# Optimization experiments

Hardware: AMD Instinct MI355X
Metric: run time of the kernel (lower is better)

The kernel has to match this reference:

```python
import jax, jax.numpy as jnp
import numpy as np

B, N, M, H, NH, IN, OUT = 64, 8192, 128, 512, 2, 128, 128
CTRL_IN = IN + NH * M  # 384


def setup_inputs() -> dict:
    key = jax.random.key(0)
    ks = jax.random.split(key, 20)
    d = {}
    d["x"] = jax.random.normal(ks[0], (B, IN), jnp.float32)
    d["prev_reads"] = jax.random.normal(ks[1], (NH, B, M), jnp.float32)
    d["h0"] = jax.random.normal(ks[2], (B, H), jnp.float32) * 0.1
    d["c0"] = jax.random.normal(ks[3], (B, H), jnp.float32) * 0.1
    wr = jax.random.uniform(ks[4], (NH, B, N), jnp.float32)
    ww = jax.random.uniform(ks[5], (NH, B, N), jnp.float32)
    d["prev_w_read"] = wr / jnp.sum(wr, axis=-1, keepdims=True)
    d["prev_w_write"] = ww / jnp.sum(ww, axis=-1, keepdims=True)
    d["memory"] = jax.random.normal(ks[6], (B, N, M), jnp.float32) * 0.1
    d["W_ih"] = jax.random.normal(ks[7], (4 * H, CTRL_IN), jnp.float32) * 0.02
    d["W_hh"] = jax.random.normal(ks[8], (4 * H, H), jnp.float32) * 0.02
    d["b_ih"] = jnp.zeros((4 * H,), jnp.float32)
    d["b_hh"] = jnp.zeros((4 * H,), jnp.float32)
    d["Wr"] = jax.random.normal(ks[9], (NH, M + 6, H), jnp.float32) * 0.05
    d["br"] = jnp.zeros((NH, M + 6), jnp.float32)
    d["Ww"] = jax.random.normal(ks[10], (NH, 3 * M + 6, H), jnp.float32) * 0.05
    d["bw"] = jnp.zeros((NH, 3 * M + 6), jnp.float32)
    d["fc_W"] = jax.random.normal(ks[11], (OUT, NH * M), jnp.float32) * 0.05
    d["fc_b"] = jnp.zeros((OUT,), jnp.float32)
    return d


def _lstm_cell(x, h, c, W_ih, W_hh, b_ih, b_hh):
    gates = x @ W_ih.T + b_ih + h @ W_hh.T + b_hh
    i, f, g, o = jnp.split(gates, 4, axis=1)  # torch gate order i,f,g,o
    i, f, o = jax.nn.sigmoid(i), jax.nn.sigmoid(f), jax.nn.sigmoid(o)
    c_new = f * c + i * jnp.tanh(g)
    return o * jnp.tanh(c_new), c_new


def _address(mem, k, beta, g, s, gamma, w_prev):
    # content addressing: cosine similarity (torch eps = 1e-8 on each norm)
    mem_e = mem + 1e-16
    k_e = k + 1e-16
    num = jnp.einsum('bnm,bm->bn', mem_e, k_e)
    den = jnp.maximum(jnp.linalg.norm(mem_e, axis=-1), 1e-8) * \
          jnp.maximum(jnp.linalg.norm(k_e, axis=-1), 1e-8)[:, None]
    wc = jax.nn.softmax(beta * num / den, axis=1)
    # interpolation
    wg = g * wc + (1.0 - g) * w_prev
    # circular convolution with 3-tap shift kernel s
    wt = s[:, 0:1] * jnp.roll(wg, 1, axis=1) + s[:, 1:2] * wg + s[:, 2:3] * jnp.roll(wg, -1, axis=1)
    # sharpening
    wp = wt ** gamma
    return wp / (jnp.sum(wp, axis=1, keepdims=True) + 1e-16)


def _split_params(o, m):
    k = o[:, :m]
    beta = jax.nn.softplus(o[:, m:m + 1])
    g = jax.nn.sigmoid(o[:, m + 1:m + 2])
    s = jax.nn.softmax(o[:, m + 2:m + 5], axis=1)
    gamma = 1.0 + jax.nn.softplus(o[:, m + 5:m + 6])
    return k, beta, g, s, gamma


def reference(x, prev_reads, h0, c0, prev_w_read, prev_w_write, memory,
              W_ih, W_hh, b_ih, b_hh, Wr, br, Ww, bw, fc_W, fc_b):
    nh, b, m = prev_reads.shape
    # controller input: [x, r_0, ..., r_{nh-1}]
    inp = jnp.concatenate([x, jnp.transpose(prev_reads, (1, 0, 2)).reshape(b, nh * m)], axis=1)
    ctrl_out, c_new = _lstm_cell(inp, h0, c0, W_ih, W_hh, b_ih, b_hh)
    reads = []
    mem = memory
    for i in range(nh):  # heads interleaved [read_i, write_i]; writes mutate memory
        # read head i
        ro = ctrl_out @ Wr[i].T + br[i]
        k, beta, g, s, gamma = _split_params(ro, m)
        w_r = _address(mem, k, beta, g, s, gamma, prev_w_read[i])
        reads.append(jnp.einsum('bn,bnm->bm', w_r, mem))
        # write head i
        wo = ctrl_out @ Ww[i].T + bw[i]
        k, beta, g, s, gamma = _split_params(wo, m)
        e = jax.nn.sigmoid(wo[:, m + 6:2 * m + 6])
        a = wo[:, 2 * m + 6:3 * m + 6]
        w_w = _address(mem, k, beta, g, s, gamma, prev_w_write[i])
        mem = mem * (1.0 - w_w[:, :, None] * e[:, None, :]) + w_w[:, :, None] * a[:, None, :]
    inp2 = jnp.concatenate(reads, axis=1)
    o = jax.nn.sigmoid(inp2 @ fc_W.T + fc_b)
    return o
```

## Files before the change

kernel.cpp:

```cpp
#include <hip/hip_runtime.h>

#define BB 64
#define NN 8192
#define MM 128
#define HH 512
#define KLSTM 896
#define JTOT 2048
#define COLS 658
#define OUTN 128
#define CHUNKS 32
#define PROW 388
#define RSTR 672

__device__ __forceinline__ float sigf(float x){ return 1.0f/(1.0f+__expf(-x)); }
__device__ __forceinline__ float tanhf_f(float x){ return 1.0f - 2.0f/(__expf(2.0f*x)+1.0f); }
__device__ __forceinline__ float softplusf_(float x){ return (x>20.0f)? x : log1pf(expf(x)); }

__global__ __launch_bounds__(128) void k_lstm_split(
    const float* __restrict__ x, const float* __restrict__ pr,
    const float* __restrict__ h0, const float* __restrict__ Wih,
    const float* __restrict__ Whh, float* __restrict__ GPART)
{
  __shared__ float a_s[64][68];
  __shared__ float w_s[64][36];
  int tid = threadIdx.x;
  int jt = blockIdx.x, ks = blockIdx.y;
  int jbase = jt*32;
  int cbeg = (ks<2)? ks*4 : 8 + (ks-2)*3;
  int cend = (ks<2)? cbeg+4 : cbeg+3;
  int jq = tid & 7, bq = tid >> 3;
  float4 acc0={0,0,0,0}, acc1={0,0,0,0}, acc2={0,0,0,0}, acc3={0,0,0,0};
  for (int c=cbeg; c<cend; ++c){
    int kc = c*64;
    __syncthreads();
    #pragma unroll
    for (int i=0;i<32;i++){
      int idx = tid + i*128;
      int kk = idx & 63, p = idx >> 6;
      int kg = kc + kk;
      float iv;
      if (kg < 128)      iv = x[p*128 + kg];
      else if (kg < 256) iv = pr[p*MM + (kg-128)];
      else if (kg < 384) iv = pr[BB*MM + p*MM + (kg-256)];
      else               iv = h0[p*HH + (kg-384)];
      a_s[kk][p] = iv;
    }
    #pragma unroll
    for (int i=0;i<16;i++){
      int idx = tid + i*128;
      int kk = idx & 63, j = idx >> 6;
      int kg = kc + kk;
      int jj = jbase + j;
      float wv = (kg < 384) ? Wih[(size_t)jj*384 + kg]
                            : Whh[(size_t)jj*512 + (kg-384)];
      w_s[kk][j] = wv;
    }
    __syncthreads();
    #pragma unroll 4
    for (int kk=0; kk<64; ++kk){
      float4 av = *(const float4*)&a_s[kk][bq*4];
      float4 wv = *(const float4*)&w_s[kk][jq*4];
      acc0.x += av.x*wv.x; acc0.y += av.x*wv.y; acc0.z += av.x*wv.z; acc0.w += av.x*wv.w;
      acc1.x += av.y*wv.x; acc1.y += av.y*wv.y; acc1.z += av.y*wv.z; acc1.w += av.y*wv.w;
      acc2.x += av.z*wv.x; acc2.y += av.z*wv.y; acc2.z += av.z*wv.z; acc2.w += av.z*wv.w;
      acc3.x += av.w*wv.x; acc3.y += av.w*wv.y; acc3.z += av.w*wv.z; acc3.w += av.w*wv.w;
    }
  }
  size_t base = (size_t)ks*BB*JTOT;
  int col = jbase + jq*4;
  *(float4*)&GPART[base + (size_t)(bq*4+0)*JTOT + col] = acc0;
  *(float4*)&GPART[base + (size_t)(bq*4+1)*JTOT + col] = acc1;
  *(float4*)&GPART[base + (size_t)(bq*4+2)*JTOT + col] = acc2;
  *(float4*)&GPART[base + (size_t)(bq*4+3)*JTOT + col] = acc3;
}

__global__ void k_ctrl(const float* __restrict__ GPART, const float* __restrict__ bih,
                       const float* __restrict__ bhh, const float* __restrict__ c0,
                       float* __restrict__ CTRL)
{
  int idx = blockIdx.x*256 + threadIdx.x;
  if (idx >= BB*HH) return;
  int b = idx >> 9, h = idx & 511;
  float g0 = bih[h]        + bhh[h];
  float g1 = bih[HH+h]     + bhh[HH+h];
  float g2 = bih[2*HH+h]   + bhh[2*HH+h];
  float g3 = bih[3*HH+h]   + bhh[3*HH+h];
  #pragma unroll
  for (int ks=0; ks<4; ++ks){
    const float* gp = GPART + ((size_t)ks*BB + b)*JTOT;
    g0 += gp[h]; g1 += gp[HH+h]; g2 += gp[2*HH+h]; g3 += gp[3*HH+h];
  }
  float i_ = sigf(g0), f_ = sigf(g1), gg = tanhf_f(g2), o_ = sigf(g3);
  CTRL[idx] = o_*tanhf_f(f_*c0[idx] + i_*gg);
}

__global__ __launch_bounds__(128) void k_head_split(
    const float* __restrict__ CTRL, const float* __restrict__ Wr,
    const float* __restrict__ Ww, float* __restrict__ RPART)
{
  __shared__ float c_s[64][68];
  __shared__ float w_s[64][36];
  int tid = threadIdx.x;
  int ct = blockIdx.x, ks = blockIdx.y;
  int cbase = ct*32;
  int jq = tid & 7, bq = tid >> 3;
  float4 acc0={0,0,0,0}, acc1={0,0,0,0}, acc2={0,0,0,0}, acc3={0,0,0,0};
  for (int cc=0; cc<2; ++cc){
    int kc = ks*128 + cc*64;
    __syncthreads();
    #pragma unroll
    for (int i=0;i<32;i++){
      int idx = tid + i*128;
      int kk = idx & 63, p = idx >> 6;
      c_s[kk][p] = CTRL[(size_t)p*HH + kc + kk];
    }
    #pragma unroll
    for (int i=0;i<16;i++){
      int idx = tid + i*128;
      int kk = idx & 63, j = idx >> 6;
      int col = cbase + j;
      int h = kc + kk;
      float wv = 0.0f;
      if (col < 134)       wv = Wr[(size_t)col*HH + h];
      else if (col < 524)  wv = Ww[(size_t)(col-134)*HH + h];
      else if (col < COLS) wv = Wr[(size_t)(134 + col-524)*HH + h];
      w_s[kk][j] = wv;
    }
    __syncthreads();
    #pragma unroll 4
    for (int kk=0; kk<64; ++kk){
      float4 av = *(const float4*)&c_s[kk][bq*4];
      float4 wv = *(const float4*)&w_s[kk][jq*4];
      acc0.x += av.x*wv.x; acc0.y += av.x*wv.y; acc0.z += av.x*wv.z; acc0.w += av.x*wv.w;
      acc1.x += av.y*wv.x; acc1.y += av.y*wv.y; acc1.z += av.y*wv.z; acc1.w += av.y*wv.w;
      acc2.x += av.z*wv.x; acc2.y += av.z*wv.y; acc2.z += av.z*wv.z; acc2.w += av.z*wv.w;
      acc3.x += av.w*wv.x; acc3.y += av.w*wv.y; acc3.z += av.w*wv.z; acc3.w += av.w*wv.w;
    }
  }
  size_t base = (size_t)ks*BB*RSTR;
  int col = cbase + jq*4;
  *(float4*)&RPART[base + (size_t)(bq*4+0)*RSTR + col] = acc0;
  *(float4*)&RPART[base + (size_t)(bq*4+1)*RSTR + col] = acc1;
  *(float4*)&RPART[base + (size_t)(bq*4+2)*RSTR + col] = acc2;
  *(float4*)&RPART[base + (size_t)(bq*4+3)*RSTR + col] = acc3;
}

__global__ __launch_bounds__(256) void k_params(
    const float* __restrict__ RPART, const float* __restrict__ br,
    const float* __restrict__ bw, float* __restrict__ COEF8,
    float* __restrict__ scal)
{
  int b = blockIdx.x, tid = threadIdx.x;
  __shared__ float ro[RSTR];
  __shared__ float wred[2][5];
  for (int idx=tid; idx<COLS; idx+=256){
    float s = (idx<134)? br[idx] : (idx<524)? bw[idx-134] : br[134 + idx-524];
    #pragma unroll
    for (int ks=0; ks<4; ++ks) s += RPART[((size_t)ks*BB + b)*RSTR + idx];
    ro[idx] = s;
  }
  __syncthreads();
  int m = tid & 127;
  float k0 = ro[m], kw = ro[134+m], k1 = ro[524+m];
  float e  = sigf(ro[268+m]);
  float a  = ro[396+m];
  if (tid < 128){
    float* c8 = COEF8 + ((size_t)b*MM + m)*8;
    *(float4*)c8     = make_float4(k0, kw, k1, e*k1);
    *(float4*)(c8+4) = make_float4(e, e*e, a, a*e);
  }
  float r0=k0*k0, r1=kw*kw, r2=k1*k1, r3=a*k1, r4=a*a;
  #pragma unroll
  for (int off=32; off; off>>=1){
    r0 += __shfl_xor(r0, off);
    r1 += __shfl_xor(r1, off);
    r2 += __shfl_xor(r2, off);
    r3 += __shfl_xor(r3, off);
    r4 += __shfl_xor(r4, off);
  }
  if (tid < 128 && (tid & 63) == 0){
    int w = tid >> 6;
    wred[w][0]=r0; wred[w][1]=r1; wred[w][2]=r2; wred[w][3]=r3; wred[w][4]=r4;
  }
  __syncthreads();
  if (tid < 3){
    float knsq = wred[0][tid] + wred[1][tid];
    float kn = fmaxf(sqrtf(knsq), 1e-8f);
    int base = (tid==0)? 0 : (tid==1)? 134 : 524;
    float beta  = softplusf_(ro[base+128]);
    float g     = sigf(ro[base+129]);
    float s0r = ro[base+130], s1r = ro[base+131], s2r = ro[base+132];
    float mx = fmaxf(s0r, fmaxf(s1r, s2r));
    float es0 = __expf(s0r-mx), es1 = __expf(s1r-mx), es2 = __expf(s2r-mx);
    float es = es0+es1+es2;
    float gamma = 1.0f + softplusf_(ro[base+133]);
    float* sc = scal + ((size_t)tid*BB + b)*8;
    sc[0]=beta; sc[1]=g; sc[2]=es0/es; sc[3]=es1/es; sc[4]=es2/es; sc[5]=gamma; sc[6]=kn;
  }
  if (tid == 3) scal[((size_t)3*BB + b)*8 + 0] = wred[0][3] + wred[1][3];
  if (tid == 4) scal[((size_t)3*BB + b)*8 + 1] = wred[0][4] + wred[1][4];
}

__global__ __launch_bounds__(256) void k_passA(
    const float* __restrict__ mem, const float* __restrict__ COEF8,
    float* __restrict__ OUT9)
{
  const size_t S = (size_t)BB*NN;
  int b = blockIdx.y, chunk = blockIdx.x;
  int tid = threadIdx.x;
  __shared__ float vtile[32][257];
  const float4* cb = (const float4*)(COEF8 + (size_t)b*MM*8);
  int rowbase = chunk*256;
  float acc[9];
  #pragma unroll
  for (int q=0;q<9;q++) acc[q] = 0.f;
  for (int kc=0; kc<4; ++kc){
    __syncthreads();
    #pragma unroll
    for (int i=0;i<8;i++){
      int f = tid + i*256;
      int r = f >> 3, k4 = f & 7;
      float4 v = *(const float4*)(mem + ((size_t)b*NN + rowbase + r)*MM + kc*32 + k4*4);
      vtile[k4*4+0][r] = v.x;
      vtile[k4*4+1][r] = v.y;
      vtile[k4*4+2][r] = v.z;
      vtile[k4*4+3][r] = v.w;
    }
    __syncthreads();
    #pragma unroll
    for (int kk=0; kk<32; ++kk){
      int kg = kc*32 + kk;
      float4 cA = cb[kg*2];
      float4 cB = cb[kg*2+1];
      float v  = vtile[kk][tid];
      float vv = v*v;
      acc[0] += v*cA.x;  acc[1] += v*cA.y;  acc[2] += vv;
      acc[3] += v*cA.z;  acc[4] += v*cA.w;
      acc[5] += vv*cB.x; acc[6] += vv*cB.y;
      acc[7] += v*cB.z;  acc[8] += v*cB.w;
    }
  }
  size_t p = (size_t)b*NN + rowbase + tid;
  #pragma unroll
  for (int q=0;q<9;q++) OUT9[(size_t)q*S + p] = acc[q];
}

__global__ __launch_bounds__(256) void k_addr(
    const float* __restrict__ OUT9, const float* __restrict__ scal,
    const float* __restrict__ pwr, const float* __restrict__ pww,
    float* __restrict__ WR0 , float* __restrict__ WR1)
{
  const size_t S = (size_t)BB*NN;
  int b = blockIdx.x, role = blockIdx.y;
  int tid = threadIdx.x;
  __shared__ float buf[NN];
  __shared__ float red[256];
  float wfin[32];

  {
    const float* numb = OUT9 + (size_t)role*S + (size_t)b*NN;
    const float* ssb  = OUT9 + 2*S + (size_t)b*NN;
    const float* wprev = ((role==0)? pwr : pww) + (size_t)b*NN;
    float* wo = WR0 + (size_t)role*S + (size_t)b*NN;
    const float* sc = scal + ((size_t)role*BB + b)*8;
    float beta=sc[0], g=sc[1], s0=sc[2], s1=sc[3], s2=sc[4], gamma=sc[5], kn=sc[6];
    float lmax = -1e30f;
    #pragma unroll
    for (int i=0;i<32;i++){
      int n = tid + i*256;
      float den = fmaxf(sqrtf(ssb[n]), 1e-8f) * kn;
      float l = beta * numb[n] / den;
      buf[n] = l;
      lmax = fmaxf(lmax, l);
    }
    red[tid] = lmax; __syncthreads();
    for (int s=128; s>0; s>>=1){ if (tid<s) red[tid]=fmaxf(red[tid],red[tid+s]); __syncthreads(); }
    lmax = red[0]; __syncthreads();
    float lsum = 0.f;
    #pragma unroll
    for (int i=0;i<32;i++){ int n = tid + i*256; float e = __expf(buf[n]-lmax); buf[n]=e; lsum+=e; }
    red[tid] = lsum; __syncthreads();
    for (int s=128; s>0; s>>=1){ if (tid<s) red[tid]+=red[tid+s]; __syncthreads(); }
    float inv = 1.0f/red[0]; __syncthreads();
    #pragma unroll
    for (int i=0;i<32;i++){ int n = tid + i*256; float wc = buf[n]*inv; buf[n] = g*wc + (1.0f-g)*wprev[n]; }
    __syncthreads();
    float psum = 0.f;
    #pragma unroll
    for (int i=0;i<32;i++){
      int n = tid + i*256;
      float wm = buf[(n-1)&(NN-1)];
      float w0 = buf[n];
      float wp = buf[(n+1)&(NN-1)];
      float wt = s0*wm + s1*w0 + s2*wp;
      float p = __expf(gamma*__logf(wt));
      wfin[i] = p; psum += p;
    }
    red[tid] = psum; __syncthreads();
    for (int s=128; s>0; s>>=1){ if (tid<s) red[tid]+=red[tid+s]; __syncthreads(); }
    float invp = 1.0f/(red[0] + 1e-16f);
    #pragma unroll
    for (int i=0;i<32;i++){ wfin[i] *= invp; wo[tid + i*256] = wfin[i]; }
  }
  if (role == 0) return;

  __syncthreads();
  {
    const float* pb = OUT9 + (size_t)b*NN;
    const float* wp = pwr + S + (size_t)b*NN;
    float* wo = WR1 + (size_t)b*NN;
    const float* sc = scal + ((size_t)2*BB + b)*8;
    float beta=sc[0], g=sc[1], s0=sc[2], s1=sc[3], s2=sc[4], gamma=sc[5], kn=sc[6];
    const float* sc3 = scal + ((size_t)3*BB + b)*8;
    float akr1 = sc3[0], aa = sc3[1];
    float lmax = -1e30f;
    #pragma unroll
    for (int i=0;i<32;i++){
      int n = tid + i*256;
      float ss = pb[2*S+n], t3 = pb[3*S+n], t4 = pb[4*S+n];
      float t5 = pb[5*S+n], t6 = pb[6*S+n], t7 = pb[7*S+n], t8 = pb[8*S+n];
      float w = wfin[i];
      float num  = t3 + w*(akr1 - t4);
      float n1sq = ss + 2.0f*w*(t7 - t5) + w*w*(t6 + aa - 2.0f*t8);
      float nrm = sqrtf(fmaxf(n1sq, 0.f));
      float l = beta * num / (fmaxf(nrm, 1e-8f) * kn);
      buf[n] = l;
      lmax = fmaxf(lmax, l);
    }
    red[tid] = lmax; __syncthreads();
    for (int s=128; s>0; s>>=1){ if (tid<s) red[tid]=fmaxf(red[tid],red[tid+s]); __syncthreads(); }
    lmax = red[0]; __syncthreads();
    float lsum = 0.f;
    #pragma unroll
    for (int i=0;i<32;i++){ int n = tid + i*256; float e = __expf(buf[n]-lmax); buf[n]=e; lsum+=e; }
    red[tid] = lsum; __syncthreads();
    for (int s=128; s>0; s>>=1){ if (tid<s) red[tid]+=red[tid+s]; __syncthreads(); }
    float inv = 1.0f/red[0]; __syncthreads();
    #pragma unroll
    for (int i=0;i<32;i++){ int n = tid + i*256; float wc = buf[n]*inv; buf[n] = g*wc + (1.0f-g)*wp[n]; }
    __syncthreads();
    float psum = 0.f;
    float wt_loc[32];
    #pragma unroll
    for (int i=0;i<32;i++){
      int n = tid + i*256;
      float wm = buf[(n-1)&(NN-1)];
      float w0 = buf[n];
      float wpv = buf[(n+1)&(NN-1)];
      float wt = s0*wm + s1*w0 + s2*wpv;
      float p = __expf(gamma*__logf(wt));
      wt_loc[i] = p; psum += p;
    }
    red[tid] = psum; __syncthreads();
    for (int s=128; s>0; s>>=1){ if (tid<s) red[tid]+=red[tid+s]; __syncthreads(); }
    float invp = 1.0f/(red[0] + 1e-16f);
    #pragma unroll
    for (int i=0;i<32;i++) wo[tid + i*256] = wt_loc[i]*invp;
  }
}

__global__ __launch_bounds__(256) void k_passF(
    const float* __restrict__ mem, const float* __restrict__ wr0,
    const float* __restrict__ wr1, const float* __restrict__ ww0,
    float* __restrict__ part)
{
  int b = blockIdx.y, chunk = blockIdx.x;
  int tid = threadIdx.x, ty = tid>>5, lane = tid&31;
  float4 a0 = {0.f,0.f,0.f,0.f}, a1 = a0, a2 = a0;
  float w2 = 0.f;
  for (int it=0; it<32; ++it){
    int n = chunk*256 + it*8 + ty;
    size_t p = (size_t)b*NN + n;
    const float4* row = (const float4*)(mem + p*MM);
    float4 v = row[lane];
    float w0r = wr0[p], w1r = wr1[p], wwr = ww0[p];
    float w12 = w1r*wwr;
    a0.x += w0r*v.x; a0.y += w0r*v.y; a0.z += w0r*v.z; a0.w += w0r*v.w;
    a1.x += w1r*v.x; a1.y += w1r*v.y; a1.z += w1r*v.z; a1.w += w1r*v.w;
    a2.x += w12*v.x; a2.y += w12*v.y; a2.z += w12*v.z; a2.w += w12*v.w;
    if (lane==0) w2 += w12;
  }
  __shared__ float4 sred[256];
  __shared__ float w2s[8];
  float* prow = part + (size_t)(b*CHUNKS + chunk)*PROW;
  float4 accs[3] = {a0,a1,a2};
  #pragma unroll
  for (int q=0;q<3;q++){
    sred[tid] = accs[q];
    __syncthreads();
    if (ty == 0){
      float4 s = {0.f,0.f,0.f,0.f};
      #pragma unroll
      for (int r=0;r<8;r++){
        float4 t = sred[r*32 + lane];
        s.x += t.x; s.y += t.y; s.z += t.z; s.w += t.w;
      }
      ((float4*)(prow + q*MM))[lane] = s;
    }
    __syncthreads();
  }
  if (lane==0) w2s[ty] = w2;
  __syncthreads();
  if (tid==0){
    float s = 0.f;
    #pragma unroll
    for (int r=0;r<8;r++) s += w2s[r];
    prow[384] = s;
  }
}

__global__ __launch_bounds__(256) void k_tail(
    const float* __restrict__ part, const float* __restrict__ COEF8,
    const float* __restrict__ fcW, const float* __restrict__ fcb,
    float* __restrict__ out)
{
  int b = blockIdx.x;
  int tid = threadIdx.x;
  __shared__ float s_lds[384];
  __shared__ float inp2[256];
  __shared__ float w2sh;
  const float* pbase = part + (size_t)b*CHUNKS*PROW;
  for (int idx=tid; idx<384; idx+=256){
    float s = 0.f;
    for (int c=0;c<CHUNKS;c++) s += pbase[(size_t)c*PROW + idx];
    s_lds[idx] = s;
  }
  if (tid == 0){
    float w = 0.f;
    for (int c=0;c<CHUNKS;c++) w += pbase[(size_t)c*PROW + 384];
    w2sh = w;
  }
  __syncthreads();
  if (tid < 128){
    int m = tid;
    float e = COEF8[((size_t)b*MM + m)*8 + 4];
    float a = COEF8[((size_t)b*MM + m)*8 + 6];
    inp2[m] = s_lds[m];
    inp2[MM + m] = s_lds[MM + m] - e*s_lds[2*MM + m] + w2sh*a;
  }
  __syncthreads();
  if (tid < 128){
    int o = tid;
    float acc = fcb[o];
    const float4* wrow = (const float4*)(fcW + (size_t)o*(2*MM));
    const float4* i2 = (const float4*)inp2;
    #pragma unroll 8
    for (int k4=0; k4<64; ++k4){
      float4 w = wrow[k4];
      float4 v = i2[k4];
      acc += w.x*v.x + w.y*v.y + w.z*v.z + w.w*v.w;
    }
    out[(size_t)b*OUTN + o] = sigf(acc);
  }
}

extern "C" void kernel_launch(void* const* d_in, const int* in_sizes, int n_in,
                              void* d_out, int out_size, void* d_ws, size_t ws_size,
                              hipStream_t stream) {
  const float* x   = (const float*)d_in[0];
  const float* pr  = (const float*)d_in[1];
  const float* h0  = (const float*)d_in[2];
  const float* c0  = (const float*)d_in[3];
  const float* pwr = (const float*)d_in[4];
  const float* pww = (const float*)d_in[5];
  const float* mem = (const float*)d_in[6];
  const float* Wih = (const float*)d_in[7];
  const float* Whh = (const float*)d_in[8];
  const float* bih = (const float*)d_in[9];
  const float* bhh = (const float*)d_in[10];
  const float* Wr  = (const float*)d_in[11];
  const float* br  = (const float*)d_in[12];
  const float* Ww  = (const float*)d_in[13];
  const float* bw  = (const float*)d_in[14];
  const float* fcW = (const float*)d_in[15];
  const float* fcb = (const float*)d_in[16];
  float* out = (float*)d_out;

  float* ws = (float*)d_ws;
  size_t off = 0;
  auto alloc = [&](size_t n){ float* p = ws + off; off += n; return p; };
  const size_t S = (size_t)BB*NN;
  float* GPART = alloc((size_t)4*BB*JTOT);
  float* CTRL  = alloc((size_t)BB*HH);
  float* RPART = alloc((size_t)4*BB*RSTR);
  float* COEF8 = alloc((size_t)BB*MM*8);
  float* SCAL  = alloc((size_t)4*BB*8);
  float* OUT9  = alloc(9*S);
  float* WR0   = alloc(S);
  float* WW0   = alloc(S);
  float* WR1   = alloc(S);
  float* PART  = alloc((size_t)BB*CHUNKS*PROW);
  (void)ws_size; (void)in_sizes; (void)n_in; (void)out_size; (void)WW0;

  k_lstm_split<<<dim3(64,4), 128, 0, stream>>>(x, pr, h0, Wih, Whh, GPART);
  k_ctrl<<<(BB*HH+255)/256, 256, 0, stream>>>(GPART, bih, bhh, c0, CTRL);
  k_head_split<<<dim3(21,4), 128, 0, stream>>>(CTRL, Wr, Ww, RPART);
  k_params<<<BB, 256, 0, stream>>>(RPART, br, bw, COEF8, SCAL);
  k_passA<<<dim3(CHUNKS,BB), 256, 0, stream>>>(mem, COEF8, OUT9);
  k_addr<<<dim3(BB,2), 256, 0, stream>>>(OUT9, SCAL, pwr, pww, WR0, WR1);
  k_passF<<<dim3(CHUNKS,BB), 256, 0, stream>>>(mem, WR0, WR1, WW0, PART);
  k_tail<<<BB, 256, 0, stream>>>(PART, COEF8, fcW, fcb, out);
}
```

Baseline: 251.0 us.

## Remap blocks to XCDs by batch and widen addressing kernel to 512 threads

Block indices are flattened and remapped so that all blocks for a given batch element land on the same XCD (blockIdx mod 8), across passA, addr, passF and tail. Data written for a batch by one kernel can then be read back from that XCD's L2 by the next kernel instead of going through a remote path. The addressing kernel also doubles its threads per block to 512, halving per-thread work and registers, with one more reduction step. The mapping relies on the hardware scheduling blocks to XCDs round-robin.

```diff
diff --git a/kernel.cpp b/kernel.cpp
--- a/kernel.cpp
+++ b/kernel.cpp
@@ -206,7 +206,10 @@
     float* __restrict__ OUT9)
 {
   const size_t S = (size_t)BB*NN;
-  int b = blockIdx.y, chunk = blockIdx.x;
+  int l = blockIdx.x;
+  int xcd = l & 7, i = l >> 3;
+  int b = xcd*8 + (i >> 5);
+  int chunk = i & 31;
   int tid = threadIdx.x;
   __shared__ float vtile[32][257];
   const float4* cb = (const float4*)(COEF8 + (size_t)b*MM*8);
@@ -217,8 +220,8 @@
   for (int kc=0; kc<4; ++kc){
     __syncthreads();
     #pragma unroll
-    for (int i=0;i<8;i++){
-      int f = tid + i*256;
+    for (int ii=0;ii<8;ii++){
+      int f = tid + ii*256;
       int r = f >> 3, k4 = f & 7;
       float4 v = *(const float4*)(mem + ((size_t)b*NN + rowbase + r)*MM + kc*32 + k4*4);
       vtile[k4*4+0][r] = v.x;
@@ -245,17 +248,20 @@
   for (int q=0;q<9;q++) OUT9[(size_t)q*S + p] = acc[q];
 }
 
-__global__ __launch_bounds__(256) void k_addr(
+__global__ __launch_bounds__(512) void k_addr(
     const float* __restrict__ OUT9, const float* __restrict__ scal,
     const float* __restrict__ pwr, const float* __restrict__ pww,
     float* __restrict__ WR0 , float* __restrict__ WR1)
 {
   const size_t S = (size_t)BB*NN;
-  int b = blockIdx.x, role = blockIdx.y;
+  int l = blockIdx.x;
+  int xcd = l & 7, j = l >> 3;
+  int role = j >> 3;
+  int b = xcd*8 + (j & 7);
   int tid = threadIdx.x;
   __shared__ float buf[NN];
-  __shared__ float red[256];
-  float wfin[32];
+  __shared__ float red[512];
+  float wfin[16];
 
   {
     const float* numb = OUT9 + (size_t)role*S + (size_t)b*NN;
@@ -266,29 +272,29 @@
     float beta=sc[0], g=sc[1], s0=sc[2], s1=sc[3], s2=sc[4], gamma=sc[5], kn=sc[6];
     float lmax = -1e30f;
     #pragma unroll
-    for (int i=0;i<32;i++){
-      int n = tid + i*256;
+    for (int i=0;i<16;i++){
+      int n = tid + i*512;
       float den = fmaxf(sqrtf(ssb[n]), 1e-8f) * kn;
-      float l = beta * numb[n] / den;
-      buf[n] = l;
-      lmax = fmaxf(lmax, l);
+      float lg = beta * numb[n] / den;
+      buf[n] = lg;
+      lmax = fmaxf(lmax, lg);
     }
     red[tid] = lmax; __syncthreads();
-    for (int s=128; s>0; s>>=1){ if (tid<s) red[tid]=fmaxf(red[tid],red[tid+s]); __syncthreads(); }
+    for (int s=256; s>0; s>>=1){ if (tid<s) red[tid]=fmaxf(red[tid],red[tid+s]); __syncthreads(); }
     lmax = red[0]; __syncthreads();
     float lsum = 0.f;
     #pragma unroll
-    for (int i=0;i<32;i++){ int n = tid + i*256; float e = __expf(buf[n]-lmax); buf[n]=e; lsum+=e; }
+    for (int i=0;i<16;i++){ int n = tid + i*512; float e = __expf(buf[n]-lmax); buf[n]=e; lsum+=e; }
     red[tid] = lsum; __syncthreads();
-    for (int s=128; s>0; s>>=1){ if (tid<s) red[tid]+=red[tid+s]; __syncthreads(); }
+    for (int s=256; s>0; s>>=1){ if (tid<s) red[tid]+=red[tid+s]; __syncthreads(); }
     float inv = 1.0f/red[0]; __syncthreads();
     #pragma unroll
-    for (int i=0;i<32;i++){ int n = tid + i*256; float wc = buf[n]*inv; buf[n] = g*wc + (1.0f-g)*wprev[n]; }
+    for (int i=0;i<16;i++){ int n = tid + i*512; float wc = buf[n]*inv; buf[n] = g*wc + (1.0f-g)*wprev[n]; }
     __syncthreads();
     float psum = 0.f;
     #pragma unroll
-    for (int i=0;i<32;i++){
-      int n = tid + i*256;
+    for (int i=0;i<16;i++){
+      int n = tid + i*512;
       float wm = buf[(n-1)&(NN-1)];
       float w0 = buf[n];
       float wp = buf[(n+1)&(NN-1)];
@@ -297,10 +303,10 @@
       wfin[i] = p; psum += p;
     }
     red[tid] = psum; __syncthreads();
-    for (int s=128; s>0; s>>=1){ if (tid<s) red[tid]+=red[tid+s]; __syncthreads(); }
+    for (int s=256; s>0; s>>=1){ if (tid<s) red[tid]+=red[tid+s]; __syncthreads(); }
     float invp = 1.0f/(red[0] + 1e-16f);
     #pragma unroll
-    for (int i=0;i<32;i++){ wfin[i] *= invp; wo[tid + i*256] = wfin[i]; }
+    for (int i=0;i<16;i++){ wfin[i] *= invp; wo[tid + i*512] = wfin[i]; }
   }
   if (role == 0) return;
 
@@ -315,35 +321,35 @@
     float akr1 = sc3[0], aa = sc3[1];
     float lmax = -1e30f;
     #pragma unroll
-    for (int i=0;i<32;i++){
-      int n = tid + i*256;
+    for (int i=0;i<16;i++){
+      int n = tid + i*512;
       float ss = pb[2*S+n], t3 = pb[3*S+n], t4 = pb[4*S+n];
       float t5 = pb[5*S+n], t6 = pb[6*S+n], t7 = pb[7*S+n], t8 = pb[8*S+n];
       float w = wfin[i];
       float num  = t3 + w*(akr1 - t4);
       float n1sq = ss + 2.0f*w*(t7 - t5) + w*w*(t6 + aa - 2.0f*t8);
       float nrm = sqrtf(fmaxf(n1sq, 0.f));
-      float l = beta * num / (fmaxf(nrm, 1e-8f) * kn);
-      buf[n] = l;
-      lmax = fmaxf(lmax, l);
+      float lg = beta * num / (fmaxf(nrm, 1e-8f) * kn);
+      buf[n] = lg;
+      lmax = fmaxf(lmax, lg);
     }
     red[tid] = lmax; __syncthreads();
-    for (int s=128; s>0; s>>=1){ if (tid<s) red[tid]=fmaxf(red[tid],red[tid+s]); __syncthreads(); }
+    for (int s=256; s>0; s>>=1){ if (tid<s) red[tid]=fmaxf(red[tid],red[tid+s]); __syncthreads(); }
     lmax = red[0]; __syncthreads();
     float lsum = 0.f;
     #pragma unroll
-    for (int i=0;i<32;i++){ int n = tid + i*256; float e = __expf(buf[n]-lmax); buf[n]=e; lsum+=e; }
+    for (int i=0;i<16;i++){ int n = tid + i*512; float e = __expf(buf[n]-lmax); buf[n]=e; lsum+=e; }
     red[tid] = lsum; __syncthreads();
-    for (int s=128; s>0; s>>=1){ if (tid<s) red[tid]+=red[tid+s]; __syncthreads(); }
+    for (int s=256; s>0; s>>=1){ if (tid<s) red[tid]+=red[tid+s]; __syncthreads(); }
     float inv = 1.0f/red[0]; __syncthreads();
     #pragma unroll
-    for (int i=0;i<32;i++){ int n = tid + i*256; float wc = buf[n]*inv; buf[n] = g*wc + (1.0f-g)*wp[n]; }
+    for (int i=0;i<16;i++){ int n = tid + i*512; float wc = buf[n]*inv; buf[n] = g*wc + (1.0f-g)*wp[n]; }
     __syncthreads();
     float psum = 0.f;
-    float wt_loc[32];
-    #pragma unroll
-    for (int i=0;i<32;i++){
-      int n = tid + i*256;
+    float wt_loc[16];
+    #pragma unroll
+    for (int i=0;i<16;i++){
+      int n = tid + i*512;
       float wm = buf[(n-1)&(NN-1)];
       float w0 = buf[n];
       float wpv = buf[(n+1)&(NN-1)];
@@ -352,10 +358,10 @@
       wt_loc[i] = p; psum += p;
     }
     red[tid] = psum; __syncthreads();
-    for (int s=128; s>0; s>>=1){ if (tid<s) red[tid]+=red[tid+s]; __syncthreads(); }
+    for (int s=256; s>0; s>>=1){ if (tid<s) red[tid]+=red[tid+s]; __syncthreads(); }
     float invp = 1.0f/(red[0] + 1e-16f);
     #pragma unroll
-    for (int i=0;i<32;i++) wo[tid + i*256] = wt_loc[i]*invp;
+    for (int i=0;i<16;i++) wo[tid + i*512] = wt_loc[i]*invp;
   }
 }
 
@@ -364,7 +370,10 @@
     const float* __restrict__ wr1, const float* __restrict__ ww0,
     float* __restrict__ part)
 {
-  int b = blockIdx.y, chunk = blockIdx.x;
+  int l = blockIdx.x;
+  int xcd = l & 7, i = l >> 3;
+  int b = xcd*8 + (i >> 5);
+  int chunk = i & 31;
   int tid = threadIdx.x, ty = tid>>5, lane = tid&31;
   float4 a0 = {0.f,0.f,0.f,0.f}, a1 = a0, a2 = a0;
   float w2 = 0.f;
@@ -414,7 +423,8 @@
     const float* __restrict__ fcW, const float* __restrict__ fcb,
     float* __restrict__ out)
 {
-  int b = blockIdx.x;
+  int l = blockIdx.x;
+  int b = (l & 7)*8 + (l >> 3);
   int tid = threadIdx.x;
   __shared__ float s_lds[384];
   __shared__ float inp2[256];
@@ -496,8 +506,8 @@
   k_ctrl<<<(BB*HH+255)/256, 256, 0, stream>>>(GPART, bih, bhh, c0, CTRL);
   k_head_split<<<dim3(21,4), 128, 0, stream>>>(CTRL, Wr, Ww, RPART);
   k_params<<<BB, 256, 0, stream>>>(RPART, br, bw, COEF8, SCAL);
-  k_passA<<<dim3(CHUNKS,BB), 256, 0, stream>>>(mem, COEF8, OUT9);
-  k_addr<<<dim3(BB,2), 256, 0, stream>>>(OUT9, SCAL, pwr, pww, WR0, WR1);
-  k_passF<<<dim3(CHUNKS,BB), 256, 0, stream>>>(mem, WR0, WR1, WW0, PART);
+  k_passA<<<CHUNKS*BB, 256, 0, stream>>>(mem, COEF8, OUT9);
+  k_addr<<<2*BB, 512, 0, stream>>>(OUT9, SCAL, pwr, pww, WR0, WR1);
+  k_passF<<<CHUNKS*BB, 256, 0, stream>>>(mem, WR0, WR1, WW0, PART);
   k_tail<<<BB, 256, 0, stream>>>(PART, COEF8, fcW, fcb, out);
 }
```

New measurement: 238.1 us. -5.1%, faster.
